# Kernel optimization log

Measured on AMD Instinct MI355X. Metric: run time of the kernel, lower is better.

The kernel has to match this reference:

```python
import jax, jax.numpy as jnp
import numpy as np

E, D_IN, D_OUT = 8, 1024, 1024
B, S = 4, 2048

def setup_inputs() -> dict:
    key = jax.random.key(0)
    k_x, k_g, k_gb, k_w = jax.random.split(key, 4)
    x = jax.random.normal(k_x, (B, S, D_IN), dtype=jnp.float32)
    gate_w = jax.random.normal(k_g, (D_IN, E), dtype=jnp.float32) * 0.02
    gate_b = jax.random.normal(k_gb, (E,), dtype=jnp.float32) * 0.02
    expert_w = jax.random.normal(k_w, (E, D_IN, D_OUT), dtype=jnp.float32) * 0.02
    return {"x": x, "gate_w": gate_w, "gate_b": gate_b, "expert_w": expert_w}

def reference(x, gate_w, gate_b, expert_w):
    # gate: softmax over experts
    gate_score = jax.nn.softmax(x @ gate_w + gate_b, axis=-1)        # [B,S,E]
    # all-expert dense GEMM: [B,S,E,out]
    expert_out = jnp.einsum('bsi,eio->bseo', x, expert_w)
    # gate-weighted combine: [B,S,out]
    out = jnp.einsum('bse,bseo->bso', gate_score, expert_out)
    return out
```

## Files before the change

### kernel.cpp

```cpp
#include <hip/hip_runtime.h>
#include <hip/hip_bf16.h>
#include <cstdint>

#define TOKENS 8192
#define DIN 1024
#define DOUT 1024
#define NE 8

typedef __bf16 bf16;
typedef __attribute__((ext_vector_type(8))) __bf16 bf16x8;
typedef __attribute__((ext_vector_type(4))) float floatx4;
typedef __attribute__((ext_vector_type(2))) float floatx2;

__device__ __forceinline__ void async16(const void* gptr, void* lptr) {
  __builtin_amdgcn_global_load_lds(
      (const __attribute__((address_space(1))) void*)gptr,
      (__attribute__((address_space(3))) void*)lptr,
      16, 0, 0);
}

__global__ __launch_bounds__(256) void prep_kernel(
    const float* __restrict__ x, const float* __restrict__ gw,
    const float* __restrict__ gb, float* __restrict__ g,
    bf16* __restrict__ xb, const float* __restrict__ w,
    bf16* __restrict__ wt) {
  __shared__ float tile[64][65];

  if (blockIdx.x < 2048) {
    const int lane = threadIdx.x & 63;
    const int wave = threadIdx.x >> 6;
    const int t = blockIdx.x * 4 + wave;
    const float* xr = x + (size_t)t * DIN;
    bf16* xbr = xb + (size_t)t * DIN;

    float acc[NE];
#pragma unroll
    for (int e = 0; e < NE; ++e) acc[e] = 0.f;

#pragma unroll
    for (int it = 0; it < 8; ++it) {
      const int i = it * 128 + lane * 2;
      const floatx2 xv = *(const floatx2*)(xr + i);
      union { bf16 b[2]; uint32_t u; } cv;
      cv.b[0] = (bf16)xv[0]; cv.b[1] = (bf16)xv[1];
      *(uint32_t*)(xbr + i) = cv.u;
      const floatx4 w00 = *(const floatx4*)(gw + (size_t)i * NE);
      const floatx4 w01 = *(const floatx4*)(gw + (size_t)i * NE + 4);
      const floatx4 w10 = *(const floatx4*)(gw + (size_t)(i + 1) * NE);
      const floatx4 w11 = *(const floatx4*)(gw + (size_t)(i + 1) * NE + 4);
#pragma unroll
      for (int e = 0; e < 4; ++e) {
        acc[e]     += xv[0] * w00[e] + xv[1] * w10[e];
        acc[e + 4] += xv[0] * w01[e] + xv[1] * w11[e];
      }
    }
#pragma unroll
    for (int e = 0; e < NE; ++e) {
#pragma unroll
      for (int off = 32; off > 0; off >>= 1)
        acc[e] += __shfl_xor(acc[e], off, 64);
    }
    float lg[NE];
    float mx = -3.0e38f;
#pragma unroll
    for (int e = 0; e < NE; ++e) { lg[e] = acc[e] + gb[e]; mx = fmaxf(mx, lg[e]); }
    float s = 0.f;
#pragma unroll
    for (int e = 0; e < NE; ++e) { lg[e] = __expf(lg[e] - mx); s += lg[e]; }
    const float inv = 1.f / s;
    if (lane == 0) {
      floatx4 o0, o1;
#pragma unroll
      for (int e = 0; e < 4; ++e) { o0[e] = lg[e] * inv; o1[e] = lg[e + 4] * inv; }
      *(floatx4*)(g + (size_t)t * NE) = o0;
      *(floatx4*)(g + (size_t)t * NE + 4) = o1;
    }
  } else {
    const int b = blockIdx.x - 2048;
    const int e = b >> 8;
    const int i0 = ((b >> 4) & 15) * 64;
    const int o0 = (b & 15) * 64;
    const int tid = threadIdx.x;
    const int c4 = (tid & 15) * 4;
    const int r = tid >> 4;

    const float* src = w + ((size_t)e * DIN + i0) * DOUT + o0;
#pragma unroll
    for (int rr = r; rr < 64; rr += 16) {
      const floatx4 v = *(const floatx4*)(src + (size_t)rr * DOUT + c4);
      tile[rr][c4] = v[0]; tile[rr][c4 + 1] = v[1];
      tile[rr][c4 + 2] = v[2]; tile[rr][c4 + 3] = v[3];
    }
    __syncthreads();
    bf16* dst = wt + ((size_t)e * DOUT + o0) * DIN + i0;
#pragma unroll
    for (int rr = r; rr < 64; rr += 16) {
      union { bf16 b[4]; uint64_t u; } cv;
#pragma unroll
      for (int j = 0; j < 4; ++j) cv.b[j] = (bf16)tile[c4 + j][rr];
      *(uint64_t*)(dst + (size_t)rr * DIN + c4) = cv.u;
    }
  }
}

__global__ __launch_bounds__(256, 2) void moe_gemm(
    const bf16* __restrict__ xb, const bf16* __restrict__ wt,
    const float* __restrict__ g, float* __restrict__ out) {
  __shared__ __align__(16) bf16 As[128 * 64];
  __shared__ __align__(16) bf16 Bs[128 * 64];

  const int tid = threadIdx.x;
  const int bm = blockIdx.x >> 3;
  const int bn = blockIdx.x & 7;
  const int lane = tid & 63;
  const int wave = tid >> 6;
  const int wm = wave >> 1, wn = wave & 1;
  const int lr = lane & 15, lq = lane >> 4;

  const int srow = tid >> 3;
  const int scol = (((tid & 7) ^ (srow & 7)) << 3);

  const bf16* agp = xb + ((size_t)(bm * 128 + srow)) * DIN + scol;
  bf16* const alp = As + tid * 8;
  bf16* const blp = Bs + tid * 8;

  const int kx = lr & 7;

  const floatx4 fzero = {0.f, 0.f, 0.f, 0.f};
  floatx4 accF[4][4];
#pragma unroll
  for (int im = 0; im < 4; ++im)
#pragma unroll
    for (int in = 0; in < 4; ++in) accF[im][in] = fzero;

  const int tok0 = bm * 128 + wm * 64;

  for (int e = 0; e < NE; ++e) {
    const bf16* bgp = wt + ((size_t)e << 20) +
                      ((size_t)(bn * 128 + srow)) * DIN + scol;
    floatx4 accE[4][4];
#pragma unroll
    for (int im = 0; im < 4; ++im)
#pragma unroll
      for (int in = 0; in < 4; ++in) accE[im][in] = fzero;

    for (int k0 = 0; k0 < DIN; k0 += 64) {
      __syncthreads();
#pragma unroll
      for (int j = 0; j < 4; ++j) {
        async16(agp + k0 + (size_t)(32 * j) * DIN, alp + j * 2048);
        async16(bgp + k0 + (size_t)(32 * j) * DIN, blp + j * 2048);
      }
      __syncthreads();

#pragma unroll
      for (int h = 0; h < 2; ++h) {
        const int kg = ((h * 4 + lq) ^ kx) << 3;
        bf16x8 av[4], bv[4];
#pragma unroll
        for (int im = 0; im < 4; ++im)
          av[im] = *(const bf16x8*)(As + (wm * 64 + im * 16 + lr) * 64 + kg);
#pragma unroll
        for (int in = 0; in < 4; ++in)
          bv[in] = *(const bf16x8*)(Bs + (wn * 64 + in * 16 + lr) * 64 + kg);
#pragma unroll
        for (int im = 0; im < 4; ++im)
#pragma unroll
          for (int in = 0; in < 4; ++in)
            accE[im][in] = __builtin_amdgcn_mfma_f32_16x16x32_bf16(
                av[im], bv[in], accE[im][in], 0, 0, 0);
      }
    }

#pragma unroll
    for (int im = 0; im < 4; ++im) {
      float gv[4];
#pragma unroll
      for (int r = 0; r < 4; ++r)
        gv[r] = g[(size_t)(tok0 + im * 16 + lq * 4 + r) * NE + e];
#pragma unroll
      for (int in = 0; in < 4; ++in)
#pragma unroll
        for (int r = 0; r < 4; ++r)
          accF[im][in][r] += gv[r] * accE[im][in][r];
    }
  }

#pragma unroll
  for (int im = 0; im < 4; ++im)
#pragma unroll
    for (int in = 0; in < 4; ++in) {
      const int col = bn * 128 + wn * 64 + in * 16 + lr;
#pragma unroll
      for (int r = 0; r < 4; ++r)
        out[(size_t)(tok0 + im * 16 + lq * 4 + r) * DOUT + col] =
            accF[im][in][r];
    }
}

extern "C" void kernel_launch(void* const* d_in, const int* in_sizes, int n_in,
                              void* d_out, int out_size, void* d_ws,
                              size_t ws_size, hipStream_t stream) {
  const float* x  = (const float*)d_in[0];
  const float* gw = (const float*)d_in[1];
  const float* gb = (const float*)d_in[2];
  const float* w  = (const float*)d_in[3];
  float* out = (float*)d_out;

  char* ws = (char*)d_ws;
  float* g  = (float*)ws;
  bf16* xb  = (bf16*)(ws + 262144);
  bf16* wt  = (bf16*)(ws + 262144 + (size_t)TOKENS * DIN * 2);

  prep_kernel<<<4096, 256, 0, stream>>>(x, gw, gb, g, xb, w, wt);
  moe_gemm<<<512, 256, 0, stream>>>(xb, wt, g, out);
}
```

Baseline: 271.5 us.

## Fold gate weights into A fragments and accumulate all experts directly

Swaps the loop order so the K loop is outer and experts are inner. The A tile is staged once per K step and held in registers, while the B tile is reloaded for each expert with extra barriers. Each A fragment is scaled by the token's gate value and rounded back to bf16 before the MFMA, so all experts accumulate into one accumulator. This drops the per-expert accE registers and the epilogue combine, but adds per-fragment VALU scale and convert work, an extra bf16 rounding of the gated input, and B reloads that sit between barriers.

```diff
diff --git a/kernel.cpp b/kernel.cpp
--- a/kernel.cpp
+++ b/kernel.cpp
@@ -17,6 +17,21 @@
       (const __attribute__((address_space(1))) void*)gptr,
       (__attribute__((address_space(3))) void*)lptr,
       16, 0, 0);
+}
+
+__device__ __forceinline__ bf16x8 scale_frag(bf16x8 a, float s) {
+  union { bf16x8 v; uint32_t u[4]; } in, out;
+  in.v = a;
+#pragma unroll
+  for (int j = 0; j < 4; ++j) {
+    const float lo = __uint_as_float(in.u[j] << 16) * s;
+    const float hi = __uint_as_float(in.u[j] & 0xffff0000u) * s;
+    union { bf16 b; uint16_t q; } c0, c1;
+    c0.b = (bf16)lo;
+    c1.b = (bf16)hi;
+    out.u[j] = (uint32_t)c0.q | ((uint32_t)c1.q << 16);
+  }
+  return out.v;
 }
 
 __global__ __launch_bounds__(256) void prep_kernel(
@@ -121,10 +136,19 @@
   const int scol = (((tid & 7) ^ (srow & 7)) << 3);
 
   const bf16* agp = xb + ((size_t)(bm * 128 + srow)) * DIN + scol;
+  const bf16* bgp = wt + ((size_t)(bn * 128 + srow)) * DIN + scol;
   bf16* const alp = As + tid * 8;
   bf16* const blp = Bs + tid * 8;
 
   const int kx = lr & 7;
+  const int tok0 = bm * 128 + wm * 64;
+
+  float gr[NE][4];
+#pragma unroll
+  for (int e = 0; e < NE; ++e)
+#pragma unroll
+    for (int im = 0; im < 4; ++im)
+      gr[e][im] = g[(size_t)(tok0 + im * 16 + lr) * NE + e];
 
   const floatx4 fzero = {0.f, 0.f, 0.f, 0.f};
   floatx4 accF[4][4];
@@ -133,33 +157,33 @@
 #pragma unroll
     for (int in = 0; in < 4; ++in) accF[im][in] = fzero;
 
-  const int tok0 = bm * 128 + wm * 64;
-
-  for (int e = 0; e < NE; ++e) {
-    const bf16* bgp = wt + ((size_t)e << 20) +
-                      ((size_t)(bn * 128 + srow)) * DIN + scol;
-    floatx4 accE[4][4];
-#pragma unroll
-    for (int im = 0; im < 4; ++im)
-#pragma unroll
-      for (int in = 0; in < 4; ++in) accE[im][in] = fzero;
-
-    for (int k0 = 0; k0 < DIN; k0 += 64) {
-      __syncthreads();
-#pragma unroll
-      for (int j = 0; j < 4; ++j) {
-        async16(agp + k0 + (size_t)(32 * j) * DIN, alp + j * 2048);
-        async16(bgp + k0 + (size_t)(32 * j) * DIN, blp + j * 2048);
-      }
-      __syncthreads();
-
+  for (int k0 = 0; k0 < DIN; k0 += 64) {
+    __syncthreads();
+#pragma unroll
+    for (int j = 0; j < 4; ++j) {
+      async16(agp + k0 + (size_t)(32 * j) * DIN, alp + j * 2048);
+      async16(bgp + k0 + (size_t)(32 * j) * DIN, blp + j * 2048);
+    }
+    __syncthreads();
+
+    bf16x8 av[2][4];
+#pragma unroll
+    for (int h = 0; h < 2; ++h)
+#pragma unroll
+      for (int im = 0; im < 4; ++im)
+        av[h][im] = *(const bf16x8*)(
+            As + (wm * 64 + im * 16 + lr) * 64 + (((h * 4 + lq) ^ kx) << 3));
+
+#pragma unroll
+    for (int e = 0; e < NE; ++e) {
 #pragma unroll
       for (int h = 0; h < 2; ++h) {
         const int kg = ((h * 4 + lq) ^ kx) << 3;
-        bf16x8 av[4], bv[4];
+        bf16x8 avs[4];
 #pragma unroll
         for (int im = 0; im < 4; ++im)
-          av[im] = *(const bf16x8*)(As + (wm * 64 + im * 16 + lr) * 64 + kg);
+          avs[im] = scale_frag(av[h][im], gr[e][im]);
+        bf16x8 bv[4];
 #pragma unroll
         for (int in = 0; in < 4; ++in)
           bv[in] = *(const bf16x8*)(Bs + (wn * 64 + in * 16 + lr) * 64 + kg);
@@ -167,22 +191,17 @@
         for (int im = 0; im < 4; ++im)
 #pragma unroll
           for (int in = 0; in < 4; ++in)
-            accE[im][in] = __builtin_amdgcn_mfma_f32_16x16x32_bf16(
-                av[im], bv[in], accE[im][in], 0, 0, 0);
+            accF[im][in] = __builtin_amdgcn_mfma_f32_16x16x32_bf16(
+                avs[im], bv[in], accF[im][in], 0, 0, 0);
       }
-    }
-
-#pragma unroll
-    for (int im = 0; im < 4; ++im) {
-      float gv[4];
-#pragma unroll
-      for (int r = 0; r < 4; ++r)
-        gv[r] = g[(size_t)(tok0 + im * 16 + lq * 4 + r) * NE + e];
-#pragma unroll
-      for (int in = 0; in < 4; ++in)
-#pragma unroll
-        for (int r = 0; r < 4; ++r)
-          accF[im][in][r] += gv[r] * accE[im][in][r];
+      if (e < NE - 1) {
+        __syncthreads();
+#pragma unroll
+        for (int j = 0; j < 4; ++j)
+          async16(bgp + ((size_t)(e + 1) << 20) + k0 + (size_t)(32 * j) * DIN,
+                  blp + j * 2048);
+        __syncthreads();
+      }
     }
   }
 
```

New measurement: 281.5 us. 1.04x slower.
